# Kernel optimization log

Hardware: AMD Instinct MI355X
Metric: run time of the kernel (lower is better)

## Reference

```python
import jax, jax.numpy as jnp
import numpy as np

OUT_FEATURES = 4096
IN_FEATURES = 4096
GROUP_SIZE = 128


def setup_inputs() -> dict:
    key = jax.random.key(0)
    k1, k2, k3, k4, k5 = jax.random.split(key, 5)
    x = jax.random.normal(k1, (4, 2048, IN_FEATURES), dtype=jnp.float32)
    # two 4-bit codes per byte-like int32 element
    packed = jax.random.randint(k2, (OUT_FEATURES * IN_FEATURES // 2,), 0, 256, dtype=jnp.int32)
    n_groups = OUT_FEATURES * IN_FEATURES // GROUP_SIZE
    scales = jax.random.uniform(k3, (n_groups,), dtype=jnp.float32) * 0.02 + 1e-3
    offsets = jax.random.normal(k4, (n_groups,), dtype=jnp.float32) * 0.01
    bias = jax.random.normal(k5, (OUT_FEATURES,), dtype=jnp.float32)
    return {"x": x, "packed": packed, "scales": scales, "offsets": offsets, "bias": bias}


def _dequant(packed, scales, offsets):
    # unpack low/high nibbles -> int codes in [0, 15]
    low = packed & 0xF
    high = (packed >> 4) & 0xF
    codes = jnp.stack([low, high], axis=-1).reshape(-1).astype(jnp.float32)  # [out*in]
    # per-group affine dequant: w = code * scale + offset
    w = codes.reshape(-1, GROUP_SIZE) * scales[:, None] + offsets[:, None]
    return w.reshape(OUT_FEATURES, IN_FEATURES)


def reference(x, packed, scales, offsets, bias):
    weight = _dequant(packed, scales, offsets)  # [out, in]
    # F.linear: x @ W^T + b
    return jnp.einsum('bsi,oi->bso', x, weight) + bias
```

## Files before the change

kernel.cpp:

```cpp
#include <hip/hip_runtime.h>
#include <hip/hip_bf16.h>
#include <stdint.h>

#define IN_F   4096
#define OUT_F  4096
#define M_TOT  8192

typedef __bf16 bf16x8 __attribute__((ext_vector_type(8)));
typedef float  floatx4 __attribute__((ext_vector_type(4)));

__device__ __forceinline__ unsigned short f2bf_bits(float f) {
    union { float f; uint32_t u; } v; v.f = f;
    uint32_t r = v.u + 0x7FFF + ((v.u >> 16) & 1);
    return (unsigned short)(r >> 16);
}

__device__ __forceinline__ void gl_lds16(const void* g, void* l) {
    __builtin_amdgcn_global_load_lds(
        (const __attribute__((address_space(1))) void*)g,
        (__attribute__((address_space(3))) void*)l, 16, 0, 0);
}

__global__ void cvt_x_kernel(const float* __restrict__ x, ushort* __restrict__ xb) {
    int i = blockIdx.x * blockDim.x + threadIdx.x;
    float4 v = reinterpret_cast<const float4*>(x)[i];
    ushort4 o;
    o.x = f2bf_bits(v.x); o.y = f2bf_bits(v.y);
    o.z = f2bf_bits(v.z); o.w = f2bf_bits(v.w);
    reinterpret_cast<ushort4*>(xb)[i] = o;
}

__global__ void dequant_kernel(const int* __restrict__ packed,
                               const float* __restrict__ scales,
                               const float* __restrict__ offsets,
                               ushort* __restrict__ wb) {
    int i = blockIdx.x * blockDim.x + threadIdx.x;
    int4 p = reinterpret_cast<const int4*>(packed)[i];
    int g = i >> 4;
    float s = scales[g], off = offsets[g];
    uint4 ov;
    {
        int pv = p.x;
        unsigned w0 = f2bf_bits((float)(pv & 0xF) * s + off);
        unsigned w1 = f2bf_bits((float)((pv >> 4) & 0xF) * s + off);
        ov.x = w0 | (w1 << 16);
    }
    {
        int pv = p.y;
        unsigned w0 = f2bf_bits((float)(pv & 0xF) * s + off);
        unsigned w1 = f2bf_bits((float)((pv >> 4) & 0xF) * s + off);
        ov.y = w0 | (w1 << 16);
    }
    {
        int pv = p.z;
        unsigned w0 = f2bf_bits((float)(pv & 0xF) * s + off);
        unsigned w1 = f2bf_bits((float)((pv >> 4) & 0xF) * s + off);
        ov.z = w0 | (w1 << 16);
    }
    {
        int pv = p.w;
        unsigned w0 = f2bf_bits((float)(pv & 0xF) * s + off);
        unsigned w1 = f2bf_bits((float)((pv >> 4) & 0xF) * s + off);
        ov.w = w0 | (w1 << 16);
    }
    reinterpret_cast<uint4*>(wb)[i] = ov;
}

__global__ void gemm_kernel(const ushort* __restrict__ A,
                            const ushort* __restrict__ B,
                            const float* __restrict__ bias,
                            float* __restrict__ C) {
    __shared__ __align__(16) ushort As[128 * 32];
    __shared__ __align__(16) ushort Bs[128 * 32];

    const int tid  = threadIdx.x;
    const int wave = tid >> 6;
    const int lane = tid & 63;
    const int quad = lane >> 4;
    const int l16  = lane & 15;
    const int wm   = wave >> 1;
    const int wn   = wave & 1;

    const int bm = blockIdx.y;
    const int bn = blockIdx.x;

    const int c0 = tid, c1 = 256 + tid;
    const int rA0 = c0 >> 2, kA0 = (c0 & 3) << 3;
    const int rA1 = c1 >> 2, kA1 = (c1 & 3) << 3;

    const ushort* gA0 = A + (size_t)(bm * 128 + rA0) * IN_F + kA0;
    const ushort* gA1 = A + (size_t)(bm * 128 + rA1) * IN_F + kA1;
    const ushort* gB0 = B + (size_t)(bn * 128 + rA0) * IN_F + kA0;
    const ushort* gB1 = B + (size_t)(bn * 128 + rA1) * IN_F + kA1;

    char* lA0 = (char*)As + wave * 1024;
    char* lA1 = (char*)As + 4096 + wave * 1024;
    char* lB0 = (char*)Bs + wave * 1024;
    char* lB1 = (char*)Bs + 4096 + wave * 1024;

    floatx4 acc[4][4] = {};

    const int arow = wm * 64 + l16;
    const int brow = wn * 64 + l16;
    const int koff = quad * 8;

    for (int k0 = 0; k0 < IN_F; k0 += 32) {
        gl_lds16(gA0, lA0);
        gl_lds16(gA1, lA1);
        gl_lds16(gB0, lB0);
        gl_lds16(gB1, lB1);
        gA0 += 32; gA1 += 32; gB0 += 32; gB1 += 32;
        __syncthreads();

        bf16x8 af[4], bfr[4];
#pragma unroll
        for (int mi = 0; mi < 4; ++mi)
            af[mi] = *reinterpret_cast<const bf16x8*>(&As[(arow + mi * 16) * 32 + koff]);
#pragma unroll
        for (int ni = 0; ni < 4; ++ni)
            bfr[ni] = *reinterpret_cast<const bf16x8*>(&Bs[(brow + ni * 16) * 32 + koff]);

#pragma unroll
        for (int mi = 0; mi < 4; ++mi)
#pragma unroll
            for (int ni = 0; ni < 4; ++ni)
                acc[mi][ni] = __builtin_amdgcn_mfma_f32_16x16x32_bf16(
                    af[mi], bfr[ni], acc[mi][ni], 0, 0, 0);

        __syncthreads();
    }

    const float* biasp = bias + bn * 128 + wn * 64 + l16;
    float* Cp = C + (size_t)(bm * 128 + wm * 64 + quad * 4) * OUT_F + bn * 128 + wn * 64 + l16;
#pragma unroll
    for (int mi = 0; mi < 4; ++mi) {
#pragma unroll
        for (int ni = 0; ni < 4; ++ni) {
            float bv = biasp[ni * 16];
#pragma unroll
            for (int r = 0; r < 4; ++r)
                Cp[(size_t)(mi * 16 + r) * OUT_F + ni * 16] = acc[mi][ni][r] + bv;
        }
    }
}

extern "C" void kernel_launch(void* const* d_in, const int* in_sizes, int n_in,
                              void* d_out, int out_size, void* d_ws, size_t ws_size,
                              hipStream_t stream) {
    const float* x       = (const float*)d_in[0];
    const int*   packed  = (const int*)d_in[1];
    const float* scales  = (const float*)d_in[2];
    const float* offsets = (const float*)d_in[3];
    const float* bias    = (const float*)d_in[4];
    float* out = (float*)d_out;

    ushort* xb = (ushort*)d_ws;
    ushort* wb = (ushort*)((char*)d_ws + (size_t)M_TOT * IN_F * 2);

    cvt_x_kernel<<<32768, 256, 0, stream>>>(x, xb);
    dequant_kernel<<<8192, 256, 0, stream>>>(packed, scales, offsets, wb);

    dim3 grid(OUT_F / 128, M_TOT / 128);
    gemm_kernel<<<grid, 256, 0, stream>>>(xb, wb, bias, out);
}
```

Baseline: 543.1 us.

## Rewrite GEMM with 256x256 tiles, 4-stage LDS pipeline, swizzle and block remap

```diff
diff --git a/kernel.cpp b/kernel.cpp
--- a/kernel.cpp
+++ b/kernel.cpp
@@ -1,13 +1,24 @@
 #include <hip/hip_runtime.h>
-#include <hip/hip_bf16.h>
 #include <stdint.h>
 
 #define IN_F   4096
 #define OUT_F  4096
 #define M_TOT  8192
+#define BK     32
+#define NT     (IN_F / BK)
+#define BUF_B  32768
+#define NBUF   4
 
 typedef __bf16 bf16x8 __attribute__((ext_vector_type(8)));
 typedef float  floatx4 __attribute__((ext_vector_type(4)));
+
+#define WAITVM(N) asm volatile("s_waitcnt vmcnt(" #N ")" ::: "memory")
+#define FENCE_BARRIER() do {                          \
+    asm volatile("" ::: "memory");                    \
+    __builtin_amdgcn_s_barrier();                     \
+    asm volatile("" ::: "memory");                    \
+    __builtin_amdgcn_sched_barrier(0);                \
+} while (0)
 
 __device__ __forceinline__ unsigned short f2bf_bits(float f) {
     union { float f; uint32_t u; } v; v.f = f;
@@ -23,11 +34,14 @@
 
 __global__ void cvt_x_kernel(const float* __restrict__ x, ushort* __restrict__ xb) {
     int i = blockIdx.x * blockDim.x + threadIdx.x;
-    float4 v = reinterpret_cast<const float4*>(x)[i];
-    ushort4 o;
-    o.x = f2bf_bits(v.x); o.y = f2bf_bits(v.y);
-    o.z = f2bf_bits(v.z); o.w = f2bf_bits(v.w);
-    reinterpret_cast<ushort4*>(xb)[i] = o;
+    const float4* xp = reinterpret_cast<const float4*>(x);
+    float4 a = xp[2 * i], b = xp[2 * i + 1];
+    uint4 o;
+    o.x = (uint32_t)f2bf_bits(a.x) | ((uint32_t)f2bf_bits(a.y) << 16);
+    o.y = (uint32_t)f2bf_bits(a.z) | ((uint32_t)f2bf_bits(a.w) << 16);
+    o.z = (uint32_t)f2bf_bits(b.x) | ((uint32_t)f2bf_bits(b.y) << 16);
+    o.w = (uint32_t)f2bf_bits(b.z) | ((uint32_t)f2bf_bits(b.w) << 16);
+    reinterpret_cast<uint4*>(xb)[i] = o;
 }
 
 __global__ void dequant_kernel(const int* __restrict__ packed,
@@ -66,77 +80,99 @@
     reinterpret_cast<uint4*>(wb)[i] = ov;
 }
 
+__launch_bounds__(512, 2)
 __global__ void gemm_kernel(const ushort* __restrict__ A,
                             const ushort* __restrict__ B,
                             const float* __restrict__ bias,
                             float* __restrict__ C) {
-    __shared__ __align__(16) ushort As[128 * 32];
-    __shared__ __align__(16) ushort Bs[128 * 32];
+    __shared__ __align__(16) char smem[NBUF * BUF_B];
 
     const int tid  = threadIdx.x;
     const int wave = tid >> 6;
     const int lane = tid & 63;
     const int quad = lane >> 4;
     const int l16  = lane & 15;
-    const int wm   = wave >> 1;
-    const int wn   = wave & 1;
-
-    const int bm = blockIdx.y;
-    const int bn = blockIdx.x;
-
-    const int c0 = tid, c1 = 256 + tid;
-    const int rA0 = c0 >> 2, kA0 = (c0 & 3) << 3;
-    const int rA1 = c1 >> 2, kA1 = (c1 & 3) << 3;
-
-    const ushort* gA0 = A + (size_t)(bm * 128 + rA0) * IN_F + kA0;
-    const ushort* gA1 = A + (size_t)(bm * 128 + rA1) * IN_F + kA1;
-    const ushort* gB0 = B + (size_t)(bn * 128 + rA0) * IN_F + kA0;
-    const ushort* gB1 = B + (size_t)(bn * 128 + rA1) * IN_F + kA1;
-
-    char* lA0 = (char*)As + wave * 1024;
-    char* lA1 = (char*)As + 4096 + wave * 1024;
-    char* lB0 = (char*)Bs + wave * 1024;
-    char* lB1 = (char*)Bs + 4096 + wave * 1024;
-
-    floatx4 acc[4][4] = {};
-
-    const int arow = wm * 64 + l16;
-    const int brow = wn * 64 + l16;
-    const int koff = quad * 8;
-
-    for (int k0 = 0; k0 < IN_F; k0 += 32) {
-        gl_lds16(gA0, lA0);
-        gl_lds16(gA1, lA1);
-        gl_lds16(gB0, lB0);
-        gl_lds16(gB1, lB1);
-        gA0 += 32; gA1 += 32; gB0 += 32; gB1 += 32;
-        __syncthreads();
-
-        bf16x8 af[4], bfr[4];
-#pragma unroll
-        for (int mi = 0; mi < 4; ++mi)
-            af[mi] = *reinterpret_cast<const bf16x8*>(&As[(arow + mi * 16) * 32 + koff]);
+    const int wm   = wave >> 2;
+    const int wn   = wave & 3;
+
+    int id = blockIdx.y * gridDim.x + blockIdx.x;
+    id = (id & 7) * 64 + (id >> 3);
+    const int bn = id & 15;
+    const int bm = id >> 4;
+
+    const int c0 = tid, c1 = 512 + tid;
+    const int r0 = c0 >> 2, r1 = c1 >> 2;
+    const int cb0 = ((c0 & 3) << 4) ^ (((r0 >> 1) & 3) << 4);
+    const int cb1 = ((c1 & 3) << 4) ^ (((r1 >> 1) & 3) << 4);
+    const ushort* gA0 = A + (size_t)(bm * 256 + r0) * IN_F + (cb0 >> 1);
+    const ushort* gA1 = A + (size_t)(bm * 256 + r1) * IN_F + (cb1 >> 1);
+    const ushort* gB0 = B + (size_t)(bn * 256 + r0) * IN_F + (cb0 >> 1);
+    const ushort* gB1 = B + (size_t)(bn * 256 + r1) * IN_F + (cb1 >> 1);
+    const int ldsA0 = wave * 1024;
+    const int ldsA1 = 8192 + wave * 1024;
+    const int ldsB0 = 16384 + wave * 1024;
+    const int ldsB1 = 24576 + wave * 1024;
+
+    auto STAGE = [&](int t) {
+        char* base = smem + (t & (NBUF - 1)) * BUF_B;
+        const int ko = t * BK;
+        gl_lds16(gA0 + ko, base + ldsA0);
+        gl_lds16(gA1 + ko, base + ldsA1);
+        gl_lds16(gB0 + ko, base + ldsB0);
+        gl_lds16(gB1 + ko, base + ldsB1);
+    };
+
+    const int arowb = wm * 128 + l16;
+    const int browb = wn * 64 + l16;
+    const int aswz = ((arowb >> 1) & 3) << 4;
+    const int bswz = ((browb >> 1) & 3) << 4;
+    const int acol = (((quad * 16) ^ aswz) >> 1);
+    const int bcol = (((quad * 16) ^ bswz) >> 1);
+
+    floatx4 acc[8][4] = {};
+
+    auto COMPUTE = [&](int t) {
+        const ushort* bufp = (const ushort*)(smem + (t & (NBUF - 1)) * BUF_B);
+        bf16x8 af[8], bfr[4];
+#pragma unroll
+        for (int mi = 0; mi < 8; ++mi)
+            af[mi] = *reinterpret_cast<const bf16x8*>(bufp + (arowb + mi * 16) * 32 + acol);
 #pragma unroll
         for (int ni = 0; ni < 4; ++ni)
-            bfr[ni] = *reinterpret_cast<const bf16x8*>(&Bs[(brow + ni * 16) * 32 + koff]);
-
-#pragma unroll
-        for (int mi = 0; mi < 4; ++mi)
+            bfr[ni] = *reinterpret_cast<const bf16x8*>(bufp + 8192 + (browb + ni * 16) * 32 + bcol);
+        __builtin_amdgcn_s_setprio(1);
+#pragma unroll
+        for (int mi = 0; mi < 8; ++mi)
 #pragma unroll
             for (int ni = 0; ni < 4; ++ni)
                 acc[mi][ni] = __builtin_amdgcn_mfma_f32_16x16x32_bf16(
                     af[mi], bfr[ni], acc[mi][ni], 0, 0, 0);
-
-        __syncthreads();
-    }
-
-    const float* biasp = bias + bn * 128 + wn * 64 + l16;
-    float* Cp = C + (size_t)(bm * 128 + wm * 64 + quad * 4) * OUT_F + bn * 128 + wn * 64 + l16;
-#pragma unroll
-    for (int mi = 0; mi < 4; ++mi) {
+        __builtin_amdgcn_s_setprio(0);
+    };
+
+    STAGE(0); STAGE(1); STAGE(2);
+    WAITVM(8);
+    FENCE_BARRIER();
+
+#pragma unroll 1
+    for (int t = 0; t < NT - 3; ++t) {
+        STAGE(t + 3);
+        COMPUTE(t);
+        WAITVM(8);
+        FENCE_BARRIER();
+    }
+    COMPUTE(NT - 3); WAITVM(4); FENCE_BARRIER();
+    COMPUTE(NT - 2); WAITVM(0); FENCE_BARRIER();
+    COMPUTE(NT - 1);
+
+    const int ccol = bn * 256 + wn * 64 + l16;
+    const float* bp = bias + ccol;
+    float* Cp = C + (size_t)(bm * 256 + wm * 128 + quad * 4) * OUT_F + ccol;
+#pragma unroll
+    for (int mi = 0; mi < 8; ++mi) {
 #pragma unroll
         for (int ni = 0; ni < 4; ++ni) {
-            float bv = biasp[ni * 16];
+            float bv = bp[ni * 16];
 #pragma unroll
             for (int r = 0; r < 4; ++r)
                 Cp[(size_t)(mi * 16 + r) * OUT_F + ni * 16] = acc[mi][ni][r] + bv;
@@ -157,9 +193,9 @@
     ushort* xb = (ushort*)d_ws;
     ushort* wb = (ushort*)((char*)d_ws + (size_t)M_TOT * IN_F * 2);
 
-    cvt_x_kernel<<<32768, 256, 0, stream>>>(x, xb);
+    cvt_x_kernel<<<16384, 256, 0, stream>>>(x, xb);
     dequant_kernel<<<8192, 256, 0, stream>>>(packed, scales, offsets, wb);
 
-    dim3 grid(OUT_F / 128, M_TOT / 128);
-    gemm_kernel<<<grid, 256, 0, stream>>>(xb, wb, bias, out);
-}
+    dim3 grid(OUT_F / 256, M_TOT / 256);
+    gemm_kernel<<<grid, 512, 0, stream>>>(xb, wb, bias, out);
+}
```

Measured after the change: 484.5 us. 1.12x faster.
